# Optimization experiments

Hardware: AMD Instinct MI355X
Metric: run time of the kernel (lower is better)

Reference implementation:

```python
import jax, jax.numpy as jnp
import numpy as np

IN, H, T, B, HW = 2048, 512, 14, 256, 49

def setup_inputs() -> dict:
    key = jax.random.key(0)
    ks = jax.random.split(key, 10)
    s = 0.02
    return {
        "x": jax.random.normal(ks[0], (B, IN, HW), jnp.float32),
        "fixation": jax.random.randint(ks[1], (B, T), 0, HW, jnp.int64),
        # stacked gate weights, order: 0=input, 1=forget, 2=output, 3=memory
        "Wx": jax.random.normal(ks[2], (4, H, IN), jnp.float32) * s,
        "bx": jnp.zeros((4, H), jnp.float32),
        "Wh": jax.random.normal(ks[3], (4, H, H), jnp.float32) * s,
        "bh": jnp.zeros((4, H), jnp.float32),
        # peephole weights, order: 0=input_c, 1=forget_c, 2=output_c
        "Wc": jax.random.normal(ks[4], (3, H, H), jnp.float32) * s,
        "bc": jnp.zeros((3, H), jnp.float32),
        "Wd": jax.random.normal(ks[5], (1, H), jnp.float32) * s,
        "bd": jnp.zeros((1,), jnp.float32),
    }

def reference(x, fixation, Wx, bx, Wh, bh, Wc, bc, Wd, bd):
    batch, feat, hw = x.shape
    seq_len = fixation.shape[1]
    # process_lengths: padding token is index 0
    lengths = seq_len - jnp.sum(fixation == 0, axis=1)  # [B]
    # gather fixated feature columns: [B, feat, T] -> [B, T, feat]
    xg = jnp.take_along_axis(x, fixation[:, None, :], axis=2)
    xg = jnp.transpose(xg, (0, 2, 1))
    # precompute all input projections for all 4 gates: [B, T, 4, H]
    xproj = jnp.einsum('btf,ghf->btgh', xg, Wx) + bx

    def step(carry, xp):  # xp: [B, 4, H]
        h, c = carry
        hp = jnp.einsum('bk,ghk->bgh', h, Wh) + bh  # [B, 4, H]
        i = jax.nn.sigmoid(xp[:, 0] + hp[:, 0] + c @ Wc[0].T + bc[0])
        f = jax.nn.sigmoid(xp[:, 1] + hp[:, 1] + c @ Wc[1].T + bc[1])
        g = jnp.tanh(xp[:, 3] + hp[:, 3])
        next_c = f * c + i * g
        o = jax.nn.sigmoid(xp[:, 2] + hp[:, 2] + next_c @ Wc[2].T + bc[2])
        h = o * next_c
        return (h, next_c), h

    hidden = Wx.shape[1]
    init = (jnp.zeros((batch, hidden), x.dtype), jnp.zeros((batch, hidden), x.dtype))
    _, hs = jax.lax.scan(step, init, jnp.transpose(xproj, (1, 0, 2, 3)))  # [T, B, H]
    hs = jnp.transpose(hs, (1, 0, 2))  # [B, T, H]
    # crop_seq: select hidden at end of each valid sequence
    last = hs[jnp.arange(batch), lengths - 1]  # [B, H]
    return jax.nn.sigmoid(last @ Wd.T + bd)  # [B, 1]
```

## Files before the change

kernel.cpp:

```cpp
#include <hip/hip_runtime.h>
#include <cstdint>
#include <cstddef>

#define B_   256
#define T_   14
#define INF_ 2048
#define H_   512
#define HW_  49
#define NG_  2048
#define KC_  1024
#define NBLK 256

typedef __attribute__((ext_vector_type(8))) _Float16 f16x8;
typedef __attribute__((ext_vector_type(4))) float f32x4;
typedef _Float16 f16;

typedef const void __attribute__((address_space(1))) gvoid_t;
typedef void __attribute__((address_space(3))) svoid_t;

__device__ __forceinline__ void async16(const void* g, void* l) {
  __builtin_amdgcn_global_load_lds((gvoid_t*)g, (svoid_t*)l, 16, 0, 0);
}

__device__ __forceinline__ float sigm(float x) { return 1.0f / (1.0f + __expf(-x)); }

__device__ __forceinline__ float aload(const float* p) {
  return __hip_atomic_load(p, __ATOMIC_RELAXED, __HIP_MEMORY_SCOPE_AGENT);
}
__device__ __forceinline__ int aloadi(const int* p) {
  return __hip_atomic_load(p, __ATOMIC_RELAXED, __HIP_MEMORY_SCOPE_AGENT);
}
__device__ __forceinline__ unsigned long long aload64(const void* p) {
  return __hip_atomic_load((const unsigned long long*)p, __ATOMIC_RELAXED, __HIP_MEMORY_SCOPE_AGENT);
}
__device__ __forceinline__ void astore(float* p, float v) {
  __hip_atomic_store(p, v, __ATOMIC_RELAXED, __HIP_MEMORY_SCOPE_AGENT);
}
__device__ __forceinline__ void astore32(void* p, unsigned v) {
  __hip_atomic_store((unsigned*)p, v, __ATOMIC_RELAXED, __HIP_MEMORY_SCOPE_AGENT);
}
__device__ __forceinline__ void astorei(int* p, int v) {
  __hip_atomic_store(p, v, __ATOMIC_RELAXED, __HIP_MEMORY_SCOPE_AGENT);
}

__device__ __forceinline__ void waitSlots(const int* slots, const int target) {
  const int* p = slots + (threadIdx.x & 31);
  for (;;) {
    const int v = aloadi(p);
    if (__all(v >= target)) break;
    __builtin_amdgcn_s_sleep(1);
  }
}

__global__ __launch_bounds__(256) void k_prep_gather(
    const float* __restrict__ Wx, const float* __restrict__ bx,
    const float* __restrict__ Wh, const float* __restrict__ Wc,
    const float* __restrict__ bh, const float* __restrict__ bc,
    const int* __restrict__ fix, const float* __restrict__ x,
    f16* __restrict__ Wxh, float* __restrict__ bxp,
    f16* __restrict__ Wbig, f16* __restrict__ Wc2h,
    float* __restrict__ biasb, f16* __restrict__ xg, int* __restrict__ tlast)
{
  const int bid = blockIdx.x;
  const int tid = threadIdx.x;
  if (bid < 1024) {
    __shared__ float rows[256 * 49];
    __shared__ int wv[T_];
    __shared__ int anyS;
    const int b = bid >> 2, part = bid & 3;
    int a = 0;
    for (int i = tid; i < B_ * T_; i += 256) a |= fix[2 * i + 1];
    if (tid == 0) anyS = 0;
    __syncthreads();
    if (a) anyS = 1;
    __syncthreads();
    const int is64 = (anyS == 0);
    if (tid < T_) wv[tid] = is64 ? fix[2 * (b * T_ + tid)] : fix[b * T_ + tid];
    __syncthreads();
    if (part == 0 && tid == 0) {
      int cnt = 0;
      for (int t = 0; t < T_; ++t) cnt += (wv[t] == 0);
      tlast[b] = (cnt < T_) ? (T_ - 1 - cnt) : (T_ - 1);
    }
    const float* xb = x + (size_t)b * (INF_ * HW_);
    for (int c = 0; c < 2; ++c) {
      const int ch = part * 2 + c;
      if (c) __syncthreads();
      const float4* src = (const float4*)(xb + (size_t)ch * 256 * 49);
      float4* dst4 = (float4*)rows;
      for (int i = tid; i < 3136; i += 256) dst4[i] = src[i];
      __syncthreads();
#pragma unroll
      for (int t = 0; t < T_; ++t)
        xg[(size_t)(b * T_ + t) * INF_ + ch * 256 + tid] = (f16)rows[tid * 49 + wv[t]];
    }
  } else {
    const int tid2 = (bid - 1024) * 256 + tid;
    const int nth = 512 * 256;
    for (int i = tid2; i < 4 * H_ * INF_; i += nth) {
      const int n = i >> 11, k = i & 2047;
      const int g = n & 3, h = n >> 2;
      Wxh[i] = (f16)Wx[((size_t)(g * H_ + h)) * INF_ + k];
    }
    for (int i = tid2; i < NG_ * KC_; i += nth) {
      const int n = i >> 10, k = i & 1023;
      const int g = n & 3, h = n >> 2;
      float v;
      if (k < H_) v = Wh[((size_t)(g * H_ + h)) * H_ + k];
      else {
        const int kk = k - H_;
        v = (g == 0) ? Wc[h * H_ + kk] : (g == 1) ? Wc[H_ * H_ + h * H_ + kk] : 0.0f;
      }
      Wbig[i] = (f16)v;
    }
    for (int i = tid2; i < H_ * H_; i += nth) Wc2h[i] = (f16)Wc[2 * H_ * H_ + i];
    for (int i = tid2; i < NG_; i += nth) {
      const int g = i & 3, h = i >> 2;
      biasb[i] = bh[g * H_ + h] + ((g == 0) ? bc[h] : (g == 1) ? bc[H_ + h] : 0.0f);
      bxp[i] = bx[g * H_ + h];
    }
  }
}

__global__ __launch_bounds__(256) void k_gemm_big(
    const f16* __restrict__ A, const f16* __restrict__ Bw,
    const float* __restrict__ bxp, float* __restrict__ Cproj)
{
  __shared__ alignas(16) f16 As[128 * 64];
  __shared__ alignas(16) f16 Bs[128 * 64];
  const int tid = threadIdx.x;
  const int lane = tid & 63;
  const int w = tid >> 6;
  const int wm = w >> 1, wn = w & 1;
  const int flat = blockIdx.y * 16 + blockIdx.x;
  const int wg = (flat & 7) * 56 + (flat >> 3);
  const int m0 = (wg >> 4) * 128, n0 = (wg & 15) * 128;
  f32x4 acc[4][4] = {};
  const int lrow = lane >> 3;
  const int kg = lane & 7;
  for (int ks = 0; ks < 2048; ks += 64) {
#pragma unroll
    for (int q = 0; q < 4; ++q) {
      const int chunk = (w << 2) + q;
      const int row = (chunk << 3) + lrow;
      const int skg = kg ^ (row & 7);
      async16(A + (size_t)(m0 + row) * 2048 + ks + (skg << 3), As + chunk * 512);
      async16(Bw + (size_t)(n0 + row) * 2048 + ks + (skg << 3), Bs + chunk * 512);
    }
    __syncthreads();
#pragma unroll
    for (int kk = 0; kk < 2; ++kk) {
      const int kgl = (kk << 2) + (lane >> 4);
      f16x8 af[4], bf[4];
#pragma unroll
      for (int mi = 0; mi < 4; ++mi) {
        const int r = (wm << 6) + (mi << 4) + (lane & 15);
        af[mi] = *(const f16x8*)(As + r * 64 + ((kgl ^ (r & 7)) << 3));
      }
#pragma unroll
      for (int ni = 0; ni < 4; ++ni) {
        const int r = (wn << 6) + (ni << 4) + (lane & 15);
        bf[ni] = *(const f16x8*)(Bs + r * 64 + ((kgl ^ (r & 7)) << 3));
      }
#pragma unroll
      for (int mi = 0; mi < 4; ++mi)
#pragma unroll
        for (int ni = 0; ni < 4; ++ni)
          acc[mi][ni] = __builtin_amdgcn_mfma_f32_16x16x32_f16(af[mi], bf[ni], acc[mi][ni], 0, 0, 0);
    }
    __syncthreads();
  }
#pragma unroll
  for (int mi = 0; mi < 4; ++mi)
#pragma unroll
    for (int ni = 0; ni < 4; ++ni)
#pragma unroll
      for (int r4 = 0; r4 < 4; ++r4) {
        const int row = m0 + (wm << 6) + (mi << 4) + ((lane >> 4) << 2) + r4;
        const int col = n0 + (wn << 6) + (ni << 4) + (lane & 15);
        Cproj[(size_t)row * 2048 + col] = acc[mi][ni][r4] + bxp[col];
      }
}

__global__ __launch_bounds__(256, 1) void k_recur(
    const f16* __restrict__ Wbig, const f16* __restrict__ Wc2h,
    const float* __restrict__ biasb, const float* __restrict__ bc,
    const float* __restrict__ xproj, f16* __restrict__ h16,
    f16* __restrict__ cb16, float* __restrict__ lasth,
    const int* __restrict__ tlast, const float* __restrict__ Wd,
    const float* __restrict__ bd, float* __restrict__ out,
    int* __restrict__ bar)
{
  __shared__ alignas(16) f16 hT[2][16 * 512];
  __shared__ alignas(16) f16 cT[2][16 * 512];
  __shared__ alignas(16) float exCN[256];
  __shared__ alignas(16) float exGO[2][256];
  __shared__ alignas(16) float ex2[4 * 256];
  const int tid = threadIdx.x, lane = tid & 63, w = tid >> 6;
  const int lk = lane >> 4;
  const int bid = blockIdx.x;
  const int pair = bid >> 5, grank = bid & 31;
  const int n0A = grank * 64, n0h = grank * 16;
  const int m0t[2] = {pair * 32, pair * 32 + 16};
  int* const sl[2] = {bar + (2 * pair) * 64, bar + (2 * pair + 1) * 64};

  f16x8 wG[32];
  {
    const f16* src = Wbig + (size_t)(n0A + w * 16 + (lane & 15)) * 1024 + (lk << 3);
#pragma unroll
    for (int kc = 0; kc < 32; ++kc) wG[kc] = *(const f16x8*)(src + kc * 32);
  }
  f16x8 wO[4];
  {
    const f16* src = Wc2h + (size_t)(n0h + (lane & 15)) * 512 + (lk << 3);
#pragma unroll
    for (int j = 0; j < 4; ++j) wO[j] = *(const f16x8*)(src + (w * 4 + j) * 32);
  }
  const int hq = (lane >> 2) & 3;
  const int browA = (lk << 2) + (lane & 3);
  const int hlA = w * 4 + hq;
  const float4 b4c = *(const float4*)(biasb + 4 * (n0h + hlA));
  const int rowB = tid >> 4, colB = tid & 15;
  const float bco = bc[1024 + n0h + colB];
  const int tlB[2] = {tlast[m0t[0] + rowB], tlast[m0t[1] + rowB]};
  {
    const f16x8 z = {};
#pragma unroll
    for (int j = 0; j < 8; ++j) *(f16x8*)(&cT[0][0] + (((j << 8) + tid) << 3)) = z;
  }
  float creg[2] = {0.f, 0.f};
  __syncthreads();

  for (int t = 0; t < T_; ++t) {
    float4 x4p[2];
#pragma unroll
    for (int tt = 0; tt < 2; ++tt)
      x4p[tt] = *(const float4*)(xproj + (size_t)((m0t[tt] + browA) * T_ + t) * 2048 +
                                 4 * (n0h + hlA));

#pragma unroll
    for (int tt = 0; tt < 2; ++tt) {
      if (t) waitSlots(sl[tt], 2 * t);
#pragma unroll
      for (int j = 0; j < 4; ++j) {
        const int u = (j << 8) + tid;
        const int row = u >> 6, kg = u & 63;
        const f16* src = h16 + (size_t)(m0t[tt] + row) * 512 + (kg << 3);
        union { f16x8 v; unsigned long long q[2]; } u2;
        u2.q[0] = aload64(src);
        u2.q[1] = aload64(src + 4);
        *(f16x8*)(&hT[tt][0] + row * 512 + ((kg >> 3) << 6) + (((kg & 7) ^ (row & 7)) << 3)) = u2.v;
      }
      __syncthreads();
      f32x4 acc[2] = {};
      {
        const int ra = lane & 15;
#pragma unroll
        for (int kc = 0; kc < 32; ++kc) {
          const int kgl = ((kc & 1) << 2) + lk;
          const f16* base = (kc < 16) ? (&hT[tt][0] + ((kc >> 1) << 6))
                                      : (&cT[tt][0] + (((kc - 16) >> 1) << 6));
          const f16x8 af = *(const f16x8*)(base + ra * 512 + ((kgl ^ (ra & 7)) << 3));
          acc[kc & 1] = __builtin_amdgcn_mfma_f32_16x16x32_f16(af, wG[kc], acc[kc & 1], 0, 0, 0);
        }
      }
      {
        const f32x4 a = acc[0] + acc[1];
        float a0 = a[0], a1 = a[1], a2 = a[2], a3 = a[3];
        {
          const bool odd = lane & 1;
          float xx = odd ? a0 : a1, yy = odd ? a2 : a3;
          xx = __shfl_xor(xx, 1); yy = __shfl_xor(yy, 1);
          if (odd) { a0 = xx; a2 = yy; } else { a1 = xx; a3 = yy; }
        }
        {
          const bool hi = lane & 2;
          float xx = hi ? a0 : a2, yy = hi ? a1 : a3;
          xx = __shfl_xor(xx, 2); yy = __shfl_xor(yy, 2);
          if (hi) { a0 = xx; a1 = yy; } else { a2 = xx; a3 = yy; }
        }
        const float gi = a0 + b4c.x + x4p[tt].x;
        const float gf = a1 + b4c.y + x4p[tt].y;
        const float go = a2 + b4c.z + x4p[tt].z;
        const float gm = a3 + b4c.w + x4p[tt].w;
        const float cn = sigm(gi) * tanhf(gm) + sigm(gf) * creg[tt];
        creg[tt] = cn;
        exCN[browA * 16 + hlA] = cn;
        exGO[tt][browA * 16 + hlA] = go;
      }
      __syncthreads();
      if (tid < 128) {
        const int rowe = tid >> 3, pr = tid & 7;
        const float2 cp = *(const float2*)(exCN + rowe * 16 + (pr << 1));
        union { unsigned u; f16 h2[2]; } pk;
        pk.h2[0] = (f16)cp.x; pk.h2[1] = (f16)cp.y;
        astore32(cb16 + (size_t)(m0t[tt] + rowe) * 512 + n0h + (pr << 1), pk.u);
      }
      __syncthreads();
      if (tid == 0)
        astorei(sl[tt] + grank, 2 * t + 1);
    }

#pragma unroll
    for (int tt = 0; tt < 2; ++tt) {
      waitSlots(sl[tt], 2 * t + 1);
#pragma unroll
      for (int j = 0; j < 4; ++j) {
        const int u = (j << 8) + tid;
        const int row = u >> 6, kg = u & 63;
        const f16* src = cb16 + (size_t)(m0t[tt] + row) * 512 + (kg << 3);
        union { f16x8 v; unsigned long long q[2]; } u2;
        u2.q[0] = aload64(src);
        u2.q[1] = aload64(src + 4);
        *(f16x8*)(&cT[tt][0] + row * 512 + ((kg >> 3) << 6) + (((kg & 7) ^ (row & 7)) << 3)) = u2.v;
      }
      __syncthreads();
      f32x4 accB = {};
      {
        const int ra = lane & 15;
#pragma unroll
        for (int j = 0; j < 4; ++j) {
          const int kc = w * 4 + j;
          const int kgl = ((kc & 1) << 2) + lk;
          const f16x8 af = *(const f16x8*)(&cT[tt][0] + ra * 512 + ((kc >> 1) << 6) +
                                           ((kgl ^ (ra & 7)) << 3));
          accB = __builtin_amdgcn_mfma_f32_16x16x32_f16(af, wO[j], accB, 0, 0, 0);
        }
      }
#pragma unroll
      for (int r4 = 0; r4 < 4; ++r4)
        ex2[w * 256 + ((lk << 2) + r4) * 16 + (lane & 15)] = accB[r4];
      __syncthreads();
      {
        const int ib = rowB * 16 + colB;
        const float sum = (ex2[ib] + ex2[256 + ib]) + (ex2[512 + ib] + ex2[768 + ib]);
        const int cg = n0h + colB;
        const float cn = (float)cT[tt][rowB * 512 + ((cg >> 6) << 6) +
                                       ((((cg >> 3) & 7) ^ (rowB & 7)) << 3) + (cg & 7)];
        const float hv = sigm(sum + exGO[tt][ib] + bco) * cn;
        const float hvo = __shfl_xor(hv, 1);
        if (!(tid & 1)) {
          union { unsigned u; f16 h2[2]; } pk;
          pk.h2[0] = (f16)hv; pk.h2[1] = (f16)hvo;
          astore32(h16 + (size_t)(m0t[tt] + rowB) * 512 + (cg & ~1), pk.u);
        }
        if (t == tlB[tt]) astore(lasth + (size_t)(m0t[tt] + rowB) * 512 + cg, hv);
      }
      __syncthreads();
      if (tid == 0)
        astorei(sl[tt] + grank, 2 * t + 2);
    }
  }

  waitSlots(sl[0], 2 * T_);
  waitSlots(sl[1], 2 * T_);
  if (w == 0) {
    const int b = pair * 32 + grank;
    float s = 0.f;
#pragma unroll
    for (int k = lane; k < 512; k += 64) s += aload(lasth + (size_t)b * 512 + k) * Wd[k];
#pragma unroll
    for (int off = 32; off > 0; off >>= 1) s += __shfl_down(s, off);
    if (lane == 0) out[b] = 1.0f / (1.0f + __expf(-(s + bd[0])));
  }
}

extern "C" void kernel_launch(void* const* d_in, const int* in_sizes, int n_in,
                              void* d_out, int out_size, void* d_ws, size_t ws_size,
                              hipStream_t stream) {
  const float* x   = (const float*)d_in[0];
  const int*   fix = (const int*)d_in[1];
  const float* Wx  = (const float*)d_in[2];
  const float* bx  = (const float*)d_in[3];
  const float* Wh  = (const float*)d_in[4];
  const float* bh  = (const float*)d_in[5];
  const float* Wc  = (const float*)d_in[6];
  const float* bc  = (const float*)d_in[7];
  const float* Wd  = (const float*)d_in[8];
  const float* bd  = (const float*)d_in[9];
  float* out = (float*)d_out;
  char* ws = (char*)d_ws;

  f16*   xg    = (f16*)(ws);
  f16*   Wxh   = (f16*)(ws + 14680064);
  float* xproj = (float*)(ws + 23068672);
  f16*   Wbig  = (f16*)(ws + 52428800);
  f16*   Wc2h  = (f16*)(ws + 56623104);
  float* biasb = (float*)(ws + 57147392);
  float* bxp   = (float*)(ws + 57155584);
  f16*   h16   = (f16*)(ws + 57163776);
  f16*   cb16  = (f16*)(ws + 57425920);
  float* lasth = (float*)(ws + 57688064);
  int*   tlast = (int*)(ws + 58212352);
  int*   bar   = (int*)(ws + 58213376);

  hipMemsetAsync(h16, 0, 262144, stream);
  hipMemsetAsync(cb16, 0, 262144, stream);
  hipMemsetAsync(bar, 0, 8192, stream);

  k_prep_gather<<<1536, 256, 0, stream>>>(Wx, bx, Wh, Wc, bh, bc, fix, x,
                                          Wxh, bxp, Wbig, Wc2h, biasb, xg, tlast);
  k_gemm_big<<<dim3(16, 28), 256, 0, stream>>>(xg, Wxh, bxp, xproj);
  k_recur<<<NBLK, 256, 0, stream>>>(Wbig, Wc2h, biasb, bc, xproj, h16, cb16,
                                    lasth, tlast, Wd, bd, out, bar);
}
```

Before: 218.4 us.

## Replace slot barriers with per-word tagged flags in recurrent exchange

```diff
diff --git a/kernel.cpp b/kernel.cpp
--- a/kernel.cpp
+++ b/kernel.cpp
@@ -14,6 +14,7 @@
 typedef __attribute__((ext_vector_type(8))) _Float16 f16x8;
 typedef __attribute__((ext_vector_type(4))) float f32x4;
 typedef _Float16 f16;
+typedef unsigned long long u64;
 
 typedef const void __attribute__((address_space(1))) gvoid_t;
 typedef void __attribute__((address_space(3))) svoid_t;
@@ -30,14 +31,14 @@
 __device__ __forceinline__ int aloadi(const int* p) {
   return __hip_atomic_load(p, __ATOMIC_RELAXED, __HIP_MEMORY_SCOPE_AGENT);
 }
-__device__ __forceinline__ unsigned long long aload64(const void* p) {
-  return __hip_atomic_load((const unsigned long long*)p, __ATOMIC_RELAXED, __HIP_MEMORY_SCOPE_AGENT);
+__device__ __forceinline__ u64 aload64(const void* p) {
+  return __hip_atomic_load((const u64*)p, __ATOMIC_RELAXED, __HIP_MEMORY_SCOPE_AGENT);
 }
 __device__ __forceinline__ void astore(float* p, float v) {
   __hip_atomic_store(p, v, __ATOMIC_RELAXED, __HIP_MEMORY_SCOPE_AGENT);
 }
-__device__ __forceinline__ void astore32(void* p, unsigned v) {
-  __hip_atomic_store((unsigned*)p, v, __ATOMIC_RELAXED, __HIP_MEMORY_SCOPE_AGENT);
+__device__ __forceinline__ void astore64(void* p, u64 v) {
+  __hip_atomic_store((u64*)p, v, __ATOMIC_RELAXED, __HIP_MEMORY_SCOPE_AGENT);
 }
 __device__ __forceinline__ void astorei(int* p, int v) {
   __hip_atomic_store(p, v, __ATOMIC_RELAXED, __HIP_MEMORY_SCOPE_AGENT);
@@ -185,15 +186,14 @@
 __global__ __launch_bounds__(256, 1) void k_recur(
     const f16* __restrict__ Wbig, const f16* __restrict__ Wc2h,
     const float* __restrict__ biasb, const float* __restrict__ bc,
-    const float* __restrict__ xproj, f16* __restrict__ h16,
-    f16* __restrict__ cb16, float* __restrict__ lasth,
+    const float* __restrict__ xproj, u64* __restrict__ hTag,
+    u64* __restrict__ cbTag, float* __restrict__ lasth,
     const int* __restrict__ tlast, const float* __restrict__ Wd,
     const float* __restrict__ bd, float* __restrict__ out,
     int* __restrict__ bar)
 {
   __shared__ alignas(16) f16 hT[2][16 * 512];
   __shared__ alignas(16) f16 cT[2][16 * 512];
-  __shared__ alignas(16) float exCN[256];
   __shared__ alignas(16) float exGO[2][256];
   __shared__ alignas(16) float ex2[4 * 256];
   const int tid = threadIdx.x, lane = tid & 63, w = tid >> 6;
@@ -202,7 +202,7 @@
   const int pair = bid >> 5, grank = bid & 31;
   const int n0A = grank * 64, n0h = grank * 16;
   const int m0t[2] = {pair * 32, pair * 32 + 16};
-  int* const sl[2] = {bar + (2 * pair) * 64, bar + (2 * pair + 1) * 64};
+  int* const slF = bar + pair * 32;
 
   f16x8 wG[32];
   {
@@ -240,16 +240,34 @@
 
 #pragma unroll
     for (int tt = 0; tt < 2; ++tt) {
-      if (t) waitSlots(sl[tt], 2 * t);
-#pragma unroll
-      for (int j = 0; j < 4; ++j) {
-        const int u = (j << 8) + tid;
-        const int row = u >> 6, kg = u & 63;
-        const f16* src = h16 + (size_t)(m0t[tt] + row) * 512 + (kg << 3);
-        union { f16x8 v; unsigned long long q[2]; } u2;
-        u2.q[0] = aload64(src);
-        u2.q[1] = aload64(src + 4);
-        *(f16x8*)(&hT[tt][0] + row * 512 + ((kg >> 3) << 6) + (((kg & 7) ^ (row & 7)) << 3)) = u2.v;
+      {
+        u64 v[16];
+        const u64* sp[16];
+        int rowc[4], kgc[4];
+        const unsigned etag = (unsigned)(2 * t);
+#pragma unroll
+        for (int c = 0; c < 4; ++c) {
+          const int u = (c << 8) + tid;
+          rowc[c] = u >> 6; kgc[c] = u & 63;
+          const u64* base = hTag + (size_t)(m0t[tt] + rowc[c]) * 256 + (kgc[c] << 2);
+#pragma unroll
+          for (int q = 0; q < 4; ++q) { sp[c * 4 + q] = base + q; v[c * 4 + q] = aload64(sp[c * 4 + q]); }
+        }
+        bool ok = false;
+        while (!ok) {
+          ok = true;
+#pragma unroll
+          for (int i = 0; i < 16; ++i)
+            if ((unsigned)(v[i] >> 32) != etag) { v[i] = aload64(sp[i]); ok = false; }
+        }
+#pragma unroll
+        for (int c = 0; c < 4; ++c) {
+          union { f16x8 g; unsigned uu[4]; } ag;
+#pragma unroll
+          for (int q = 0; q < 4; ++q) ag.uu[q] = (unsigned)v[c * 4 + q];
+          *(f16x8*)(&hT[tt][0] + rowc[c] * 512 + ((kgc[c] >> 3) << 6) +
+                    (((kgc[c] & 7) ^ (rowc[c] & 7)) << 3)) = ag.g;
+        }
       }
       __syncthreads();
       f32x4 acc[2] = {};
@@ -285,34 +303,47 @@
         const float gm = a3 + b4c.w + x4p[tt].w;
         const float cn = sigm(gi) * tanhf(gm) + sigm(gf) * creg[tt];
         creg[tt] = cn;
-        exCN[browA * 16 + hlA] = cn;
         exGO[tt][browA * 16 + hlA] = go;
-      }
-      __syncthreads();
-      if (tid < 128) {
-        const int rowe = tid >> 3, pr = tid & 7;
-        const float2 cp = *(const float2*)(exCN + rowe * 16 + (pr << 1));
-        union { unsigned u; f16 h2[2]; } pk;
-        pk.h2[0] = (f16)cp.x; pk.h2[1] = (f16)cp.y;
-        astore32(cb16 + (size_t)(m0t[tt] + rowe) * 512 + n0h + (pr << 1), pk.u);
-      }
-      __syncthreads();
-      if (tid == 0)
-        astorei(sl[tt] + grank, 2 * t + 1);
+        const float cnP = __shfl_xor(cn, 4);
+        if (!(lane & 4)) {
+          union { unsigned u; f16 h2[2]; } pk;
+          pk.h2[0] = (f16)cn; pk.h2[1] = (f16)cnP;
+          astore64(cbTag + (size_t)(m0t[tt] + browA) * 256 + (grank << 3) + (w << 1) + (hq >> 1),
+                   ((u64)(unsigned)(2 * t + 1) << 32) | pk.u);
+        }
+      }
     }
 
 #pragma unroll
     for (int tt = 0; tt < 2; ++tt) {
-      waitSlots(sl[tt], 2 * t + 1);
-#pragma unroll
-      for (int j = 0; j < 4; ++j) {
-        const int u = (j << 8) + tid;
-        const int row = u >> 6, kg = u & 63;
-        const f16* src = cb16 + (size_t)(m0t[tt] + row) * 512 + (kg << 3);
-        union { f16x8 v; unsigned long long q[2]; } u2;
-        u2.q[0] = aload64(src);
-        u2.q[1] = aload64(src + 4);
-        *(f16x8*)(&cT[tt][0] + row * 512 + ((kg >> 3) << 6) + (((kg & 7) ^ (row & 7)) << 3)) = u2.v;
+      {
+        u64 v[16];
+        const u64* sp[16];
+        int rowc[4], kgc[4];
+        const unsigned etag = (unsigned)(2 * t + 1);
+#pragma unroll
+        for (int c = 0; c < 4; ++c) {
+          const int u = (c << 8) + tid;
+          rowc[c] = u >> 6; kgc[c] = u & 63;
+          const u64* base = cbTag + (size_t)(m0t[tt] + rowc[c]) * 256 + (kgc[c] << 2);
+#pragma unroll
+          for (int q = 0; q < 4; ++q) { sp[c * 4 + q] = base + q; v[c * 4 + q] = aload64(sp[c * 4 + q]); }
+        }
+        bool ok = false;
+        while (!ok) {
+          ok = true;
+#pragma unroll
+          for (int i = 0; i < 16; ++i)
+            if ((unsigned)(v[i] >> 32) != etag) { v[i] = aload64(sp[i]); ok = false; }
+        }
+#pragma unroll
+        for (int c = 0; c < 4; ++c) {
+          union { f16x8 g; unsigned uu[4]; } ag;
+#pragma unroll
+          for (int q = 0; q < 4; ++q) ag.uu[q] = (unsigned)v[c * 4 + q];
+          *(f16x8*)(&cT[tt][0] + rowc[c] * 512 + ((kgc[c] >> 3) << 6) +
+                    (((kgc[c] & 7) ^ (rowc[c] & 7)) << 3)) = ag.g;
+        }
       }
       __syncthreads();
       f32x4 accB = {};
@@ -342,18 +373,18 @@
         if (!(tid & 1)) {
           union { unsigned u; f16 h2[2]; } pk;
           pk.h2[0] = (f16)hv; pk.h2[1] = (f16)hvo;
-          astore32(h16 + (size_t)(m0t[tt] + rowB) * 512 + (cg & ~1), pk.u);
+          astore64(hTag + (size_t)(m0t[tt] + rowB) * 256 + (grank << 3) + (colB >> 1),
+                   ((u64)(unsigned)(2 * t + 2) << 32) | pk.u);
         }
         if (t == tlB[tt]) astore(lasth + (size_t)(m0t[tt] + rowB) * 512 + cg, hv);
       }
-      __syncthreads();
-      if (tid == 0)
-        astorei(sl[tt] + grank, 2 * t + 2);
-    }
-  }
-
-  waitSlots(sl[0], 2 * T_);
-  waitSlots(sl[1], 2 * T_);
+    }
+  }
+
+  asm volatile("s_waitcnt vmcnt(0)" ::: "memory");
+  __syncthreads();
+  if (tid == 0) astorei(slF + grank, 1);
+  waitSlots(slF, 1);
   if (w == 0) {
     const int b = pair * 32 + grank;
     float s = 0.f;
@@ -388,19 +419,19 @@
   f16*   Wc2h  = (f16*)(ws + 56623104);
   float* biasb = (float*)(ws + 57147392);
   float* bxp   = (float*)(ws + 57155584);
-  f16*   h16   = (f16*)(ws + 57163776);
-  f16*   cb16  = (f16*)(ws + 57425920);
-  float* lasth = (float*)(ws + 57688064);
-  int*   tlast = (int*)(ws + 58212352);
-  int*   bar   = (int*)(ws + 58213376);
-
-  hipMemsetAsync(h16, 0, 262144, stream);
-  hipMemsetAsync(cb16, 0, 262144, stream);
+  u64*   hTag  = (u64*)(ws + 57163776);
+  u64*   cbTag = (u64*)(ws + 57688064);
+  float* lasth = (float*)(ws + 58212352);
+  int*   tlast = (int*)(ws + 58736640);
+  int*   bar   = (int*)(ws + 58737664);
+
+  hipMemsetAsync(hTag, 0, 524288, stream);
+  hipMemsetAsync(cbTag, 0, 524288, stream);
   hipMemsetAsync(bar, 0, 8192, stream);
 
   k_prep_gather<<<1536, 256, 0, stream>>>(Wx, bx, Wh, Wc, bh, bc, fix, x,
                                           Wxh, bxp, Wbig, Wc2h, biasb, xg, tlast);
   k_gemm_big<<<dim3(16, 28), 256, 0, stream>>>(xg, Wxh, bxp, xproj);
-  k_recur<<<NBLK, 256, 0, stream>>>(Wbig, Wc2h, biasb, bc, xproj, h16, cb16,
+  k_recur<<<NBLK, 256, 0, stream>>>(Wbig, Wc2h, biasb, bc, xproj, hTag, cbTag,
                                     lasth, tlast, Wd, bd, out, bar);
 }
```

Result: no change. 221.7 us (+1.5%).
